# Optimization experiments

Hardware: AMD Instinct MI355X
Metric: run time of the kernel (lower is better)

Reference implementation:

```python
import jax, jax.numpy as jnp
import numpy as np

B, T, N, C = 1, 8, 1152, 768
H, DH = 12, 64          # attention heads / head dim; also RG-LRU block-diagonal heads
MLP = 3072
LRU = 768
CONV_W = 4              # recurrentgemma temporal conv width
N_IMG = 1024            # image tokens blocked by mask_image2image


def rms_norm(x, scale):
    var = jnp.mean(jnp.square(x), axis=-1, keepdims=True)
    return x * jax.lax.rsqrt(var + 1e-6) * (1.0 + scale)


def layer_norm(x, scale, bias):
    m = jnp.mean(x, axis=-1, keepdims=True)
    v = jnp.var(x, axis=-1, keepdims=True)
    return (x - m) * jax.lax.rsqrt(v + 1e-6) * scale + bias


def block_diag_linear(x, w, b):
    # x [..., LRU] -> per-head block-diagonal linear (recurrentgemma BlockDiagonalLinear)
    xs = x.reshape(x.shape[:-1] + (H, DH))
    y = jnp.einsum('...hd,hde->...he', xs, w) + b
    return y.reshape(x.shape)


def setup_inputs():
    key = jax.random.key(0)
    ks = jax.random.split(key, 24)
    def nrm(k, shape, s=0.02):
        return jax.random.normal(k, shape, jnp.float32) * s
    return dict(
        x=jax.random.normal(ks[0], (B, T, N, C), jnp.float32),
        tpre_scale=nrm(ks[1], (C,)),
        w_y=nrm(ks[2], (C, LRU)), b_y=jnp.zeros((LRU,)),
        w_x=nrm(ks[3], (C, LRU)), b_x=jnp.zeros((LRU,)),
        conv_w=nrm(ks[4], (CONV_W, LRU)), conv_b=jnp.zeros((LRU,)),
        a_param=jax.random.uniform(ks[5], (LRU,), jnp.float32, 1.0, 4.0),
        ig_w=nrm(ks[6], (H, DH, DH)), ig_b=jnp.zeros((H, DH)),
        ag_w=nrm(ks[7], (H, DH, DH)), ag_b=jnp.zeros((H, DH)),
        w_out=nrm(ks[8], (LRU, C)), b_out=jnp.zeros((C,)),
        cpre_scale=nrm(ks[9], (C,)),
        ffw_up_w=nrm(ks[10], (2, C, MLP)), ffw_up_b=jnp.zeros((2, MLP)),
        ffw_down_w=nrm(ks[11], (MLP, C)), ffw_down_b=jnp.zeros((C,)),
        ln1_s=jnp.ones((C,)), ln1_b=jnp.zeros((C,)),
        wq=nrm(ks[12], (C, H, DH)), bq=jnp.zeros((H, DH)),
        wk=nrm(ks[13], (C, H, DH)), bk=jnp.zeros((H, DH)),
        wv=nrm(ks[14], (C, H, DH)), bv=jnp.zeros((H, DH)),
        wo=nrm(ks[15], (H, DH, C)), bo=jnp.zeros((C,)),
        ln2_s=jnp.ones((C,)), ln2_b=jnp.zeros((C,)),
        mlp_w1=nrm(ks[16], (C, MLP)), mlp_b1=jnp.zeros((MLP,)),
        mlp_w2=nrm(ks[17], (MLP, C)), mlp_b2=jnp.zeros((C,)),
    )


def forward(x, tpre_scale, w_y, b_y, w_x, b_x, conv_w, conv_b, a_param,
            ig_w, ig_b, ag_w, ag_b, w_out, b_out, cpre_scale,
            ffw_up_w, ffw_up_b, ffw_down_w, ffw_down_b,
            ln1_s, ln1_b, wq, bq, wk, bk, wv, bv, wo, bo,
            ln2_s, ln2_b, mlp_w1, mlp_b1, mlp_w2, mlp_b2):
    b, t, n, c = x.shape
    # ---- temporal RG-LRU residual block over time: [(b t) n c] -> [(b n) t c] ----
    xt = x.transpose(0, 2, 1, 3).reshape(b * n, t, c)
    raw = xt
    xn = rms_norm(xt, tpre_scale)
    y = jax.nn.gelu(xn @ w_y + b_y)              # gate branch
    u = xn @ w_x + b_x                           # recurrent branch
    # causal depthwise temporal conv (width 4)
    up = jnp.pad(u, ((0, 0), (CONV_W - 1, 0), (0, 0)))
    u = sum(conv_w[i] * up[:, i:i + t] for i in range(CONV_W)) + conv_b
    # RG-LRU
    gate_x = jax.nn.sigmoid(block_diag_linear(u, ig_w, ig_b))
    gate_a = jax.nn.sigmoid(block_diag_linear(u, ag_w, ag_b))
    log_a = -8.0 * gate_a * jax.nn.softplus(a_param)
    a = jnp.exp(log_a)                           # [bn, t, LRU]
    mult = jnp.sqrt(jnp.maximum(1.0 - jnp.exp(2.0 * log_a), 0.0))
    reset = (jnp.arange(t) == 0)[None, :, None]
    mult = jnp.where(reset, 1.0, mult)
    a = jnp.where(reset, 0.0, a)
    norm_x = u * gate_x * mult
    def step(h, inputs):
        a_t, x_t = inputs
        h = a_t * h + x_t
        return h, h
    _, hs = jax.lax.scan(step, jnp.zeros((b * n, LRU), u.dtype),
                         (a.transpose(1, 0, 2), norm_x.transpose(1, 0, 2)))
    h = hs.transpose(1, 0, 2)                    # [bn, t, LRU]
    s = (h * y) @ w_out + b_out
    resid = s + raw
    # gated MLP (recurrentgemma MLPBlock)
    z = rms_norm(resid, cpre_scale)
    up2 = jnp.einsum('btd,cdD->cbtD', z, ffw_up_w) + ffw_up_b[:, None, None, :]
    z = (jax.nn.gelu(up2[0]) * up2[1]) @ ffw_down_w + ffw_down_b
    xt = z + resid
    # ---- spatial ViT block over tokens: back to [(b t) n c] ----
    xs = xt.reshape(b, n, t, c).transpose(0, 2, 1, 3).reshape(b * t, n, c)
    y1 = layer_norm(xs, ln1_s, ln1_b)
    q = jnp.einsum('bnc,chd->bnhd', y1, wq) + bq
    k = jnp.einsum('bnc,chd->bnhd', y1, wk) + bk
    v = jnp.einsum('bnc,chd->bnhd', y1, wv) + bv
    logits = jnp.einsum('bqhd,bkhd->bhqk', q, k) / jnp.sqrt(jnp.asarray(DH, q.dtype))
    # mask_image2image: image tokens (first 1024) cannot attend to image tokens
    mask = jnp.ones((n, n), bool).at[:N_IMG, :N_IMG].set(False)
    logits = jnp.where(mask[None, None], logits, jnp.finfo(logits.dtype).min)
    attn = jax.nn.softmax(logits, axis=-1)
    sa = jnp.einsum('bhqk,bkhd->bqhd', attn, v)
    sa = jnp.einsum('bqhd,hdc->bqc', sa, wo) + bo
    xs = xs + sa
    y2 = layer_norm(xs, ln2_s, ln2_b)
    m = jax.nn.gelu(y2 @ mlp_w1 + mlp_b1) @ mlp_w2 + mlp_b2
    xs = xs + m
    return xs.reshape(b, t, n, c)


def reference(x, tpre_scale, w_y, b_y, w_x, b_x, conv_w, conv_b, a_param,
              ig_w, ig_b, ag_w, ag_b, w_out, b_out, cpre_scale,
              ffw_up_w, ffw_up_b, ffw_down_w, ffw_down_b,
              ln1_s, ln1_b, wq, bq, wk, bk, wv, bv, wo, bo,
              ln2_s, ln2_b, mlp_w1, mlp_b1, mlp_w2, mlp_b2):
    return forward(x, tpre_scale, w_y, b_y, w_x, b_x, conv_w, conv_b, a_param,
                   ig_w, ig_b, ag_w, ag_b, w_out, b_out, cpre_scale,
                   ffw_up_w, ffw_up_b, ffw_down_w, ffw_down_b,
                   ln1_s, ln1_b, wq, bq, wk, bk, wv, bv, wo, bo,
                   ln2_s, ln2_b, mlp_w1, mlp_b1, mlp_w2, mlp_b2)
```

## Files before the change

### kernel.cpp

```cpp
#include <hip/hip_runtime.h>
#include <hip/hip_bf16.h>

typedef __hip_bfloat16 bf16;
typedef __attribute__((ext_vector_type(4))) float f32x4;
typedef __attribute__((ext_vector_type(8))) short short8;

#define T_ 8
#define N_ 1152
#define C_ 768
#define H_ 12
#define DH_ 64
#define MLP_ 3072
#define LRU_ 768
#define NIMG_ 1024
#define M_ (T_*N_)

__device__ __forceinline__ float b2f(bf16 v){ return __bfloat162float(v); }
__device__ __forceinline__ bf16  f2b(float f){ return __float2bfloat16(f); }
__device__ __forceinline__ float gelu_tanh(float x){
  float x3 = x*x*x;
  float z = 1.5957691216057308f*(x + 0.044715f*x3);
  float e = __expf(z);
  float t = 1.f - 2.f/(e + 1.f);
  return 0.5f*x*(1.f + t);
}
__device__ __forceinline__ void gll16(const void* g, void* l) {
  __builtin_amdgcn_global_load_lds((const __attribute__((address_space(1))) void*)g,
                                   (__attribute__((address_space(3))) void*)l, 16, 0, 0);
}
__device__ __forceinline__ f32x4 mfma16(short8 a, short8 b, f32x4 c) {
  return __builtin_amdgcn_mfma_f32_16x16x32_bf16(a, b, c, 0, 0, 0);
}

__global__ __launch_bounds__(256)
void convertT(const float* __restrict__ W, bf16* __restrict__ Wt, int Kd, int Nd,
              int rs, int ro) {
  __shared__ float tile[64][65];
  int k0 = blockIdx.y * 64, n0 = blockIdx.x * 64;
  int tid = threadIdx.x;
  int c = tid & 63, rr = tid >> 6;
  #pragma unroll
  for (int i = 0; i < 16; i++) {
    int r = rr * 16 + i;
    tile[r][c] = W[(size_t)(k0 + r) * Nd + n0 + c];
  }
  __syncthreads();
  #pragma unroll
  for (int i = 0; i < 16; i++) {
    int n = rr * 16 + i;
    Wt[(size_t)((n0 + n) * rs + ro) * Kd + k0 + c] = f2b(tile[c][n]);
  }
}

__global__ __launch_bounds__(256)
void convert_gw(const float* __restrict__ igw, const float* __restrict__ agw,
                const float* __restrict__ igb, const float* __restrict__ agb,
                bf16* __restrict__ GW, float* __restrict__ GB) {
  int h = blockIdx.x;
  for (int idx = threadIdx.x; idx < 128 * 64; idx += 256) {
    int rowc = idx >> 6;
    int d    = idx & 63;
    int e    = rowc >> 1;
    const float* W = (rowc & 1) ? agw : igw;
    GW[((size_t)h * 128 + rowc) * 64 + d] = f2b(W[((size_t)h * 64 + d) * 64 + e]);
  }
  if (threadIdx.x < 128) {
    int rowc = threadIdx.x;
    GB[h * 128 + rowc] = ((rowc & 1) ? agb : igb)[h * 64 + (rowc >> 1)];
  }
}

template<int EPI, int ACT>
__global__ __launch_bounds__(256)
void mgemm(const bf16* __restrict__ A, const bf16* __restrict__ Wt,
           const float* __restrict__ bias, const float* __restrict__ resid,
           void* __restrict__ outp, int K, int Nd) {
  __shared__ bf16 As[2][128][32];
  __shared__ bf16 Bs[2][128][32];
  int tid = threadIdx.x;
  int wave = tid >> 6, lane = tid & 63;
  int wm = wave >> 1, wn = wave & 1;
  int ln15 = lane & 15, quad = lane >> 4;
  int row0 = blockIdx.y * 128, col0 = blockIdx.x * 128;
  const bf16* ag = A  + (size_t)(row0 + wave*32 + (lane>>2)) * K + (lane&3)*8;
  const bf16* bg = Wt + (size_t)(col0 + wave*32 + (lane>>2)) * K + (lane&3)*8;
  f32x4 zero = {0.f, 0.f, 0.f, 0.f};
  f32x4 acc[4][4];
  #pragma unroll
  for (int i = 0; i < 4; i++)
    #pragma unroll
    for (int j = 0; j < 4; j++) acc[i][j] = zero;

  gll16(ag,          &As[0][wave*32][0]);
  gll16(ag + 16*K,   &As[0][wave*32 + 16][0]);
  gll16(bg,          &Bs[0][wave*32][0]);
  gll16(bg + 16*K,   &Bs[0][wave*32 + 16][0]);
  __syncthreads();

  int nt = K >> 5;
  int cur = 0;
  for (int t = 0; t < nt; ++t) {
    if (t + 1 < nt) {
      int k1 = (t + 1) << 5;
      gll16(ag + k1,          &As[cur^1][wave*32][0]);
      gll16(ag + 16*K + k1,   &As[cur^1][wave*32 + 16][0]);
      gll16(bg + k1,          &Bs[cur^1][wave*32][0]);
      gll16(bg + 16*K + k1,   &Bs[cur^1][wave*32 + 16][0]);
    }
    short8 af[4], bf[4];
    #pragma unroll
    for (int i = 0; i < 4; i++)
      af[i] = *(const short8*)&As[cur][wm*64 + i*16 + ln15][quad*8];
    #pragma unroll
    for (int i = 0; i < 4; i++)
      bf[i] = *(const short8*)&Bs[cur][wn*64 + i*16 + ln15][quad*8];
    #pragma unroll
    for (int i = 0; i < 4; i++)
      #pragma unroll
      for (int j = 0; j < 4; j++)
        acc[i][j] = mfma16(af[i], bf[j], acc[i][j]);
    __syncthreads();
    cur ^= 1;
  }

  #pragma unroll
  for (int i = 0; i < 4; i++) {
    #pragma unroll
    for (int j = 0; j < 4; j++) {
      int col = col0 + wn*64 + j*16 + ln15;
      float bv = (EPI == 3) ? bias[(col & 1) * (Nd >> 1) + (col >> 1)] : bias[col];
      #pragma unroll
      for (int r = 0; r < 4; r++) {
        int row = row0 + wm*64 + i*16 + quad*4 + r;
        float v = acc[i][j][r] + bv;
        if (EPI == 3) {
          float pv = __shfl_xor(v, 1, 64);
          if ((lane & 1) == 0)
            ((bf16*)outp)[(size_t)row * (Nd >> 1) + (col >> 1)] = f2b(gelu_tanh(v) * pv);
        } else {
          if (ACT) v = gelu_tanh(v);
          if (EPI == 0) {
            ((bf16*)outp)[(size_t)row * Nd + col] = f2b(v);
          } else if (EPI == 1) {
            size_t o = (size_t)row * Nd + col;
            ((float*)outp)[o] = v + resid[o];
          } else if (EPI == 2) {
            int tt = row / N_; int nn = row - tt * N_;
            ((bf16*)outp)[(((size_t)tt * H_ + (col >> 6)) * 64 + (col & 63)) * N_ + nn] = f2b(v);
          }
        }
      }
    }
  }
}

template<int LN>
__global__ __launch_bounds__(256)
void norm_kernel(const float* __restrict__ inp, const float* __restrict__ s,
                 const float* __restrict__ b, bf16* __restrict__ out) {
  int wid  = threadIdx.x >> 6;
  int lane = threadIdx.x & 63;
  int tok  = blockIdx.x * 4 + wid;
  float v[12];
  float sum = 0.f, sq = 0.f;
  #pragma unroll
  for (int i = 0; i < 12; i++) {
    int c = lane + i * 64;
    float x = inp[(size_t)tok*C_ + c];
    v[i] = x; sum += x; sq += x * x;
  }
  #pragma unroll
  for (int o = 32; o > 0; o >>= 1) {
    sum += __shfl_xor(sum, o, 64);
    sq  += __shfl_xor(sq, o, 64);
  }
  float scale, mean = 0.f;
  if (LN) {
    mean = sum * (1.f / C_);
    float var = sq * (1.f / C_) - mean * mean;
    scale = rsqrtf(var + 1e-6f);
  } else {
    scale = rsqrtf(sq * (1.f / C_) + 1e-6f);
  }
  #pragma unroll
  for (int i = 0; i < 12; i++) {
    int c = lane + i * 64;
    float sc = s[c];
    float r;
    if (LN) r = (v[i] - mean) * scale * sc + b[c];
    else    r = v[i] * scale * (1.f + sc);
    out[(size_t)tok*C_ + c] = f2b(r);
  }
}

__global__ __launch_bounds__(256)
void conv_kernel(const bf16* __restrict__ u0, const float* __restrict__ cw,
                 const float* __restrict__ cb, bf16* __restrict__ uc) {
  int idx = blockIdx.x * 256 + threadIdx.x;
  int ch  = idx % LRU_;
  int tok = idx / LRU_;
  int n = tok % N_;
  int t = tok / N_;
  float acc = cb[ch];
  #pragma unroll
  for (int i = 0; i < 4; i++) {
    int tt = t - 3 + i;
    if (tt >= 0)
      acc += cw[i*LRU_ + ch] * b2f(u0[(size_t)(tt*N_ + n)*LRU_ + ch]);
  }
  uc[idx] = f2b(acc);
}

__global__ __launch_bounds__(256)
void gates_mfma(const bf16* __restrict__ uc, const bf16* __restrict__ GW,
                const float* __restrict__ GB, const float* __restrict__ ap,
                bf16* __restrict__ a_out, bf16* __restrict__ nx_out) {
  __shared__ bf16 As[128][64];
  __shared__ bf16 Bs[128][64];
  int tid = threadIdx.x;
  int wave = tid >> 6, lane = tid & 63;
  int wm = wave >> 1, wn = wave & 1;
  int ln15 = lane & 15, quad = lane >> 4;
  int row0 = blockIdx.x * 128;
  int h = blockIdx.y;
  #pragma unroll
  for (int i = 0; i < 4; i++) {
    int chunk = wave * 4 + i;
    gll16(uc + (size_t)(row0 + chunk*8 + (lane>>3)) * LRU_ + h*DH_ + (lane&7)*8,
          &As[chunk*8][0]);
    gll16(GW + (size_t)h*128*64 + chunk*512 + lane*8, &Bs[chunk*8][0]);
  }
  __syncthreads();
  f32x4 zero = {0.f, 0.f, 0.f, 0.f};
  f32x4 acc[4][4];
  #pragma unroll
  for (int i = 0; i < 4; i++)
    #pragma unroll
    for (int j = 0; j < 4; j++) acc[i][j] = zero;
  short8 af0[4], af1[4], bf0[4], bf1[4];
  #pragma unroll
  for (int i = 0; i < 4; i++) {
    af0[i] = *(const short8*)&As[wm*64 + i*16 + ln15][quad*8];
    af1[i] = *(const short8*)&As[wm*64 + i*16 + ln15][32 + quad*8];
    bf0[i] = *(const short8*)&Bs[wn*64 + i*16 + ln15][quad*8];
    bf1[i] = *(const short8*)&Bs[wn*64 + i*16 + ln15][32 + quad*8];
  }
  #pragma unroll
  for (int i = 0; i < 4; i++)
    #pragma unroll
    for (int j = 0; j < 4; j++) {
      acc[i][j] = mfma16(af0[i], bf0[j], acc[i][j]);
      acc[i][j] = mfma16(af1[i], bf1[j], acc[i][j]);
    }
  __syncthreads();

  int t_is0 = (row0 < N_);
  int odd = lane & 1;
  float bvj[4], spj[4];
  #pragma unroll
  for (int j = 0; j < 4; j++) {
    int col = wn*64 + j*16 + ln15;
    bvj[j] = GB[h*128 + col];
    int e = col >> 1;
    float apv = ap[h*DH_ + e];
    spj[j] = (apv > 20.f) ? apv : log1pf(__expf(apv));
  }
  #pragma unroll
  for (int i = 0; i < 4; i++) {
    #pragma unroll
    for (int j = 0; j < 4; j++) {
      int col = wn*64 + j*16 + ln15;
      int e = col >> 1;
      #pragma unroll
      for (int r = 0; r < 4; r++) {
        int lr = wm*64 + i*16 + quad*4 + r;
        float v = acc[i][j][r] + bvj[j];
        float g = 1.f / (1.f + __expf(-v));
        float mult = 1.f;
        if (odd) {
          float log_a = -8.f * g * spj[j];
          float a = __expf(log_a);
          mult = sqrtf(fmaxf(1.f - a*a, 0.f));
          if (t_is0) { a = 0.f; mult = 1.f; }
          Bs[lr][e] = f2b(a);
        }
        float mp = __shfl_xor(mult, 1, 64);
        if (!odd) {
          float uv = b2f(As[lr][e]);
          As[lr][e] = f2b(uv * g * mp);
        }
      }
    }
  }
  __syncthreads();
  int rr = tid >> 3, cc = (tid & 7) * 8;
  #pragma unroll
  for (int it = 0; it < 4; it++) {
    int row = it * 32 + rr;
    size_t o = (size_t)(row0 + row) * LRU_ + h*DH_ + cc;
    *(short8*)(nx_out + o) = *(const short8*)&As[row][cc];
    *(short8*)(a_out  + o) = *(const short8*)&Bs[row][cc];
  }
}

__global__ __launch_bounds__(256)
void scan_kernel(const bf16* __restrict__ a, const bf16* __restrict__ nx,
                 const bf16* __restrict__ y, bf16* __restrict__ hy) {
  int idx = blockIdx.x * 256 + threadIdx.x;
  int n  = idx / LRU_;
  int ch = idx % LRU_;
  float h = 0.f;
  #pragma unroll
  for (int t = 0; t < T_; t++) {
    size_t p = (size_t)(t*N_ + n) * LRU_ + ch;
    h = b2f(a[p]) * h + b2f(nx[p]);
    hy[p] = f2b(h * b2f(y[p]));
  }
}

__global__ __launch_bounds__(256)
void fattn(const bf16* __restrict__ Q, const bf16* __restrict__ Kg,
           const bf16* __restrict__ Vt, bf16* __restrict__ O) {
  __shared__ bf16 Ks[128][64];
  __shared__ bf16 VTs[64][128];
  __shared__ bf16 Ps[4][16][128];
  int qb = blockIdx.x, th = blockIdx.y;
  int h = th % H_, t = th / H_;
  int wave = threadIdx.x >> 6, lane = threadIdx.x & 63;
  int ln15 = lane & 15, quad = lane >> 4;
  int q0, kv0, nch;
  if (qb < 16) { q0 = qb * 64;            kv0 = NIMG_; nch = 1; }
  else         { q0 = NIMG_ + (qb-16)*64; kv0 = 0;     nch = 9; }
  int qw = q0 + wave * 16;
  const bf16* qp = Q + (size_t)(t*N_ + qw + ln15) * C_ + h*DH_ + quad*8;
  short8 aq0 = *(const short8*)qp;
  short8 aq1 = *(const short8*)(qp + 32);
  f32x4 zero = {0.f, 0.f, 0.f, 0.f};
  f32x4 oacc[4];
  #pragma unroll
  for (int d = 0; d < 4; d++) oacc[d] = zero;
  float mi[4], li[4];
  #pragma unroll
  for (int r = 0; r < 4; r++) { mi[r] = -1e30f; li[r] = 0.f; }

  for (int ch = 0; ch < nch; ch++) {
    int kb = t*N_ + kv0 + ch*128;
    #pragma unroll
    for (int i = 0; i < 4; i++) {
      int r = wave*32 + i*8;
      gll16(Kg + (size_t)(kb + r + (lane>>3))*C_ + h*DH_ + (lane&7)*8, &Ks[r][0]);
    }
    #pragma unroll
    for (int i = 0; i < 4; i++) {
      int d = wave*16 + i*4;
      gll16(Vt + ((size_t)(t*H_ + h)*64 + d + (lane>>4))*N_ + kv0 + ch*128 + ln15*8,
            &VTs[d][0]);
    }
    __syncthreads();
    f32x4 s[8];
    #pragma unroll
    for (int nt = 0; nt < 8; nt++) {
      short8 b0 = *(const short8*)&Ks[nt*16 + ln15][quad*8];
      short8 b1 = *(const short8*)&Ks[nt*16 + ln15][32 + quad*8];
      f32x4 c_ = zero;
      c_ = mfma16(aq0, b0, c_);
      c_ = mfma16(aq1, b1, c_);
      #pragma unroll
      for (int r = 0; r < 4; r++) s[nt][r] = c_[r] * 0.125f;
    }
    float alpha[4], lsum[4];
    #pragma unroll
    for (int r = 0; r < 4; r++) {
      float m_ = s[0][r];
      #pragma unroll
      for (int nt = 1; nt < 8; nt++) m_ = fmaxf(m_, s[nt][r]);
      #pragma unroll
      for (int o = 1; o < 16; o <<= 1) m_ = fmaxf(m_, __shfl_xor(m_, o, 64));
      float mnew = fmaxf(mi[r], m_);
      alpha[r] = __expf(mi[r] - mnew);
      mi[r] = mnew;
      lsum[r] = 0.f;
    }
    #pragma unroll
    for (int nt = 0; nt < 8; nt++)
      #pragma unroll
      for (int r = 0; r < 4; r++) {
        float p = __expf(s[nt][r] - mi[r]);
        s[nt][r] = p; lsum[r] += p;
      }
    #pragma unroll
    for (int r = 0; r < 4; r++) {
      float l_ = lsum[r];
      #pragma unroll
      for (int o = 1; o < 16; o <<= 1) l_ += __shfl_xor(l_, o, 64);
      li[r] = li[r] * alpha[r] + l_;
    }
    #pragma unroll
    for (int nt = 0; nt < 8; nt++)
      #pragma unroll
      for (int r = 0; r < 4; r++)
        Ps[wave][quad*4 + r][nt*16 + ln15] = f2b(s[nt][r]);
    #pragma unroll
    for (int d = 0; d < 4; d++)
      #pragma unroll
      for (int r = 0; r < 4; r++) oacc[d][r] *= alpha[r];
    #pragma unroll
    for (int ks = 0; ks < 4; ks++) {
      short8 pa = *(const short8*)&Ps[wave][ln15][ks*32 + quad*8];
      #pragma unroll
      for (int dt = 0; dt < 4; dt++) {
        short8 vb = *(const short8*)&VTs[dt*16 + ln15][ks*32 + quad*8];
        oacc[dt] = mfma16(pa, vb, oacc[dt]);
      }
    }
    __syncthreads();
  }
  #pragma unroll
  for (int dt = 0; dt < 4; dt++)
    #pragma unroll
    for (int r = 0; r < 4; r++)
      O[(size_t)(t*N_ + qw + quad*4 + r)*C_ + h*DH_ + dt*16 + ln15]
        = f2b(oacc[dt][r] / li[r]);
}

extern "C" void kernel_launch(void* const* d_in, const int* in_sizes, int n_in,
                              void* d_out, int out_size, void* d_ws, size_t ws_size,
                              hipStream_t stream) {
  (void)in_sizes; (void)n_in; (void)out_size; (void)ws_size;
  const float* x        = (const float*)d_in[0];
  const float* tpre     = (const float*)d_in[1];
  const float* w_y      = (const float*)d_in[2];
  const float* b_y      = (const float*)d_in[3];
  const float* w_x      = (const float*)d_in[4];
  const float* b_x      = (const float*)d_in[5];
  const float* conv_w   = (const float*)d_in[6];
  const float* conv_b   = (const float*)d_in[7];
  const float* a_param  = (const float*)d_in[8];
  const float* ig_w     = (const float*)d_in[9];
  const float* ig_b     = (const float*)d_in[10];
  const float* ag_w     = (const float*)d_in[11];
  const float* ag_b     = (const float*)d_in[12];
  const float* w_out    = (const float*)d_in[13];
  const float* b_out    = (const float*)d_in[14];
  const float* cpre     = (const float*)d_in[15];
  const float* ffw_up_w = (const float*)d_in[16];
  const float* ffw_up_b = (const float*)d_in[17];
  const float* ffw_dn_w = (const float*)d_in[18];
  const float* ffw_dn_b = (const float*)d_in[19];
  const float* ln1_s    = (const float*)d_in[20];
  const float* ln1_b    = (const float*)d_in[21];
  const float* wq       = (const float*)d_in[22];
  const float* bq       = (const float*)d_in[23];
  const float* wk       = (const float*)d_in[24];
  const float* bk       = (const float*)d_in[25];
  const float* wv       = (const float*)d_in[26];
  const float* bv       = (const float*)d_in[27];
  const float* wo       = (const float*)d_in[28];
  const float* bo       = (const float*)d_in[29];
  const float* ln2_s    = (const float*)d_in[30];
  const float* ln2_b    = (const float*)d_in[31];
  const float* mlp_w1   = (const float*)d_in[32];
  const float* mlp_b1   = (const float*)d_in[33];
  const float* mlp_w2   = (const float*)d_in[34];
  const float* mlp_b2   = (const float*)d_in[35];

  const size_t MC = (size_t)M_ * C_;
  const size_t W68 = (size_t)C_ * C_;
  const size_t WUP = (size_t)C_ * MLP_;
  bf16* B0 = (bf16*)d_ws;
  bf16* B1 = B0 + MC;
  bf16* B2 = B1 + MC;
  bf16* BV = B2 + MC;
  float* F0 = (float*)(BV + MC);
  float* F1 = F0 + MC;
  bf16* F0b = (bf16*)F0;
  bf16* B0b = (bf16*)B0;
  float* xsF = (float*)B0;
  float* outF = (float*)d_out;
  bf16*  GW = (bf16*)F1;
  float* GB = (float*)(GW + (size_t)H_*128*64);

  dim3 blk(256);
  dim3 gN768(C_/128, M_/128);
  dim3 cv768(12, 12);
  dim3 cvUp(48, 12);
  dim3 cvDn(12, 48);

  convertT<<<cv768, blk, 0, stream>>>(w_y, BV, C_, C_, 1, 0);
  convertT<<<cv768, blk, 0, stream>>>(w_x, BV + W68, C_, C_, 1, 0);
  convert_gw<<<H_, blk, 0, stream>>>(ig_w, ag_w, ig_b, ag_b, GW, GB);
  norm_kernel<0><<<M_/4, blk, 0, stream>>>(x, tpre, nullptr, B0);
  mgemm<0,1><<<gN768, blk, 0, stream>>>(B0, BV, b_y, nullptr, B1, C_, C_);
  mgemm<0,0><<<gN768, blk, 0, stream>>>(B0, BV + W68, b_x, nullptr, B2, C_, C_);
  conv_kernel<<<(M_*LRU_)/256, blk, 0, stream>>>(B2, conv_w, conv_b, B0);
  gates_mfma<<<dim3(M_/128, H_), blk, 0, stream>>>(B0, GW, GB, a_param, B2, BV);
  scan_kernel<<<(N_*LRU_)/256, blk, 0, stream>>>(B2, BV, B1, B0);
  convertT<<<cv768, blk, 0, stream>>>(w_out, BV, C_, C_, 1, 0);
  mgemm<1,0><<<gN768, blk, 0, stream>>>(B0, BV, b_out, x, outF, C_, C_);

  norm_kernel<0><<<M_/4, blk, 0, stream>>>(outF, cpre, nullptr, B0);
  convertT<<<cvUp, blk, 0, stream>>>(ffw_up_w,       B1, C_, MLP_, 2, 0);
  convertT<<<cvUp, blk, 0, stream>>>(ffw_up_w + WUP, B1, C_, MLP_, 2, 1);
  convertT<<<cvDn, blk, 0, stream>>>(ffw_dn_w, BV, MLP_, C_, 1, 0);
  {
    dim3 gUp(6144/128, M_/128);
    dim3 gDn(C_/128,   M_/128);
    mgemm<3,0><<<gUp, blk, 0, stream>>>(B0, B1, ffw_up_b, nullptr, F0b, C_, 6144);
    mgemm<1,0><<<gDn, blk, 0, stream>>>(F0b, BV, ffw_dn_b, outF, xsF, MLP_, C_);
  }

  norm_kernel<1><<<M_/4, blk, 0, stream>>>(xsF, ln1_s, ln1_b, B2);
  convertT<<<cv768, blk, 0, stream>>>(wq, BV,          C_, C_, 1, 0);
  convertT<<<cv768, blk, 0, stream>>>(wk, BV + W68,    C_, C_, 1, 0);
  convertT<<<cv768, blk, 0, stream>>>(wv, BV + 2*W68,  C_, C_, 1, 0);
  convertT<<<cv768, blk, 0, stream>>>(wo, BV + 3*W68,  C_, C_, 1, 0);
  mgemm<0,0><<<gN768, blk, 0, stream>>>(B2, BV,         bq, nullptr, F0b,        C_, C_);
  mgemm<0,0><<<gN768, blk, 0, stream>>>(B2, BV + W68,   bk, nullptr, F0b + MC,   C_, C_);
  mgemm<2,0><<<gN768, blk, 0, stream>>>(B2, BV + 2*W68, bv, nullptr, F0b + 2*MC, C_, C_);
  fattn<<<dim3(18, T_*H_), blk, 0, stream>>>(F0b, F0b + MC, F0b + 2*MC, B2);
  mgemm<1,0><<<gN768, blk, 0, stream>>>(B2, BV + 3*W68, bo, xsF, outF, C_, C_);
  norm_kernel<1><<<M_/4, blk, 0, stream>>>(outF, ln2_s, ln2_b, B2);
  convertT<<<cvUp, blk, 0, stream>>>(mlp_w1, B0b,       C_, MLP_, 1, 0);
  convertT<<<cvDn, blk, 0, stream>>>(mlp_w2, B0b + WUP, MLP_, C_, 1, 0);
  {
    dim3 gM1(MLP_/128, M_/128);
    dim3 gM2(C_/128,   M_/128);
    mgemm<0,1><<<gM1, blk, 0, stream>>>(B2, B0b, mlp_b1, nullptr, F0b, C_, MLP_);
    mgemm<1,0><<<gM2, blk, 0, stream>>>(F0b, B0b + WUP, mlp_b2, outF, outF, MLP_, C_);
  }
}
```

Measured before the change: 928.6 us.

## Fuse paired GEMMs and weight conversions, vectorize norm, conv and scan kernels

Merges the y/x projection GEMMs and the q/k projection GEMMs into single N=1536 GEMMs with a split-bias epilogue, and batches several weight transposes into one multi-job launch via blockIdx.z. Norm, conv and scan kernels now process 4 or 8 channels per thread using vector loads and stores. fattn reads Q and K from the interleaved 1536-wide buffer. This cuts launch count and improves memory coalescing, at the cost of more buffer aliasing and stride bookkeeping.

```diff
diff --git a/kernel.cpp b/kernel.cpp
--- a/kernel.cpp
+++ b/kernel.cpp
@@ -4,6 +4,7 @@
 typedef __hip_bfloat16 bf16;
 typedef __attribute__((ext_vector_type(4))) float f32x4;
 typedef __attribute__((ext_vector_type(8))) short short8;
+typedef __attribute__((ext_vector_type(4))) short s16x4;
 
 #define T_ 8
 #define N_ 1152
@@ -17,6 +18,7 @@
 
 __device__ __forceinline__ float b2f(bf16 v){ return __bfloat162float(v); }
 __device__ __forceinline__ bf16  f2b(float f){ return __float2bfloat16(f); }
+__device__ __forceinline__ float bfs(short u){ return __uint_as_float(((unsigned int)(unsigned short)u) << 16); }
 __device__ __forceinline__ float gelu_tanh(float x){
   float x3 = x*x*x;
   float z = 1.5957691216057308f*(x + 0.044715f*x3);
@@ -36,6 +38,31 @@
 void convertT(const float* __restrict__ W, bf16* __restrict__ Wt, int Kd, int Nd,
               int rs, int ro) {
   __shared__ float tile[64][65];
+  int k0 = blockIdx.y * 64, n0 = blockIdx.x * 64;
+  int tid = threadIdx.x;
+  int c = tid & 63, rr = tid >> 6;
+  #pragma unroll
+  for (int i = 0; i < 16; i++) {
+    int r = rr * 16 + i;
+    tile[r][c] = W[(size_t)(k0 + r) * Nd + n0 + c];
+  }
+  __syncthreads();
+  #pragma unroll
+  for (int i = 0; i < 16; i++) {
+    int n = rr * 16 + i;
+    Wt[(size_t)((n0 + n) * rs + ro) * Kd + k0 + c] = f2b(tile[c][n]);
+  }
+}
+
+struct CvJob  { const float* src; bf16* dst; };
+struct CvJobs { CvJob j[4]; };
+__global__ __launch_bounds__(256)
+void convertT4(CvJobs jobs, int Kd, int Nd, int rs, int zro) {
+  __shared__ float tile[64][65];
+  int z = blockIdx.z;
+  const float* __restrict__ W  = jobs.j[z].src;
+  bf16* __restrict__ Wt        = jobs.j[z].dst;
+  int ro = z * zro;
   int k0 = blockIdx.y * 64, n0 = blockIdx.x * 64;
   int tid = threadIdx.x;
   int c = tid & 63, rr = tid >> 6;
@@ -73,7 +100,7 @@
 template<int EPI, int ACT>
 __global__ __launch_bounds__(256)
 void mgemm(const bf16* __restrict__ A, const bf16* __restrict__ Wt,
-           const float* __restrict__ bias, const float* __restrict__ resid,
+           const float* __restrict__ bias, const float* __restrict__ bias2,
            void* __restrict__ outp, int K, int Nd) {
   __shared__ bf16 As[2][128][32];
   __shared__ bf16 Bs[2][128][32];
@@ -128,7 +155,10 @@
     #pragma unroll
     for (int j = 0; j < 4; j++) {
       int col = col0 + wn*64 + j*16 + ln15;
-      float bv = (EPI == 3) ? bias[(col & 1) * (Nd >> 1) + (col >> 1)] : bias[col];
+      float bv;
+      if (EPI == 3)      bv = bias[(col & 1) * (Nd >> 1) + (col >> 1)];
+      else if (EPI == 4) bv = (col < (Nd >> 1)) ? bias[col] : bias2[col - (Nd >> 1)];
+      else               bv = bias[col];
       #pragma unroll
       for (int r = 0; r < 4; r++) {
         int row = row0 + wm*64 + i*16 + quad*4 + r;
@@ -137,13 +167,16 @@
           float pv = __shfl_xor(v, 1, 64);
           if ((lane & 1) == 0)
             ((bf16*)outp)[(size_t)row * (Nd >> 1) + (col >> 1)] = f2b(gelu_tanh(v) * pv);
+        } else if (EPI == 4) {
+          if (ACT && col < (Nd >> 1)) v = gelu_tanh(v);
+          ((bf16*)outp)[(size_t)row * Nd + col] = f2b(v);
         } else {
           if (ACT) v = gelu_tanh(v);
           if (EPI == 0) {
             ((bf16*)outp)[(size_t)row * Nd + col] = f2b(v);
           } else if (EPI == 1) {
             size_t o = (size_t)row * Nd + col;
-            ((float*)outp)[o] = v + resid[o];
+            ((float*)outp)[o] = v + bias2[o];
           } else if (EPI == 2) {
             int tt = row / N_; int nn = row - tt * N_;
             ((bf16*)outp)[(((size_t)tt * H_ + (col >> 6)) * 64 + (col & 63)) * N_ + nn] = f2b(v);
@@ -161,13 +194,14 @@
   int wid  = threadIdx.x >> 6;
   int lane = threadIdx.x & 63;
   int tok  = blockIdx.x * 4 + wid;
-  float v[12];
+  const float* ip = inp + (size_t)tok*C_ + lane*4;
+  f32x4 v[3];
   float sum = 0.f, sq = 0.f;
   #pragma unroll
-  for (int i = 0; i < 12; i++) {
-    int c = lane + i * 64;
-    float x = inp[(size_t)tok*C_ + c];
-    v[i] = x; sum += x; sq += x * x;
+  for (int i = 0; i < 3; i++) {
+    v[i] = *(const f32x4*)(ip + i*256);
+    #pragma unroll
+    for (int j = 0; j < 4; j++) { sum += v[i][j]; sq += v[i][j]*v[i][j]; }
   }
   #pragma unroll
   for (int o = 32; o > 0; o >>= 1) {
@@ -183,32 +217,57 @@
     scale = rsqrtf(sq * (1.f / C_) + 1e-6f);
   }
   #pragma unroll
-  for (int i = 0; i < 12; i++) {
-    int c = lane + i * 64;
-    float sc = s[c];
-    float r;
-    if (LN) r = (v[i] - mean) * scale * sc + b[c];
-    else    r = v[i] * scale * (1.f + sc);
-    out[(size_t)tok*C_ + c] = f2b(r);
+  for (int i = 0; i < 3; i++) {
+    int c0 = i*256 + lane*4;
+    f32x4 sc = *(const f32x4*)(s + c0);
+    f32x4 bb;
+    if (LN) bb = *(const f32x4*)(b + c0);
+    bf16 tmp[4];
+    #pragma unroll
+    for (int j = 0; j < 4; j++) {
+      float r;
+      if (LN) r = (v[i][j] - mean) * scale * sc[j] + bb[j];
+      else    r = v[i][j] * scale * (1.f + sc[j]);
+      tmp[j] = f2b(r);
+    }
+    *(s16x4*)(out + (size_t)tok*C_ + c0) = *(const s16x4*)tmp;
   }
 }
 
 __global__ __launch_bounds__(256)
 void conv_kernel(const bf16* __restrict__ u0, const float* __restrict__ cw,
-                 const float* __restrict__ cb, bf16* __restrict__ uc) {
+                 const float* __restrict__ cb, bf16* __restrict__ uc, int us, int uo) {
   int idx = blockIdx.x * 256 + threadIdx.x;
-  int ch  = idx % LRU_;
-  int tok = idx / LRU_;
+  int c8  = idx % (LRU_/8);
+  int tok = idx / (LRU_/8);
+  int ch0 = c8 * 8;
   int n = tok % N_;
   int t = tok / N_;
-  float acc = cb[ch];
+  float acc[8];
+  {
+    f32x4 b0 = *(const f32x4*)(cb + ch0);
+    f32x4 b1 = *(const f32x4*)(cb + ch0 + 4);
+    #pragma unroll
+    for (int j = 0; j < 4; j++) { acc[j] = b0[j]; acc[4+j] = b1[j]; }
+  }
   #pragma unroll
   for (int i = 0; i < 4; i++) {
     int tt = t - 3 + i;
-    if (tt >= 0)
-      acc += cw[i*LRU_ + ch] * b2f(u0[(size_t)(tt*N_ + n)*LRU_ + ch]);
-  }
-  uc[idx] = f2b(acc);
+    if (tt >= 0) {
+      short8 v = *(const short8*)&u0[(size_t)(tt*N_ + n)*us + uo + ch0];
+      f32x4 w0 = *(const f32x4*)(cw + i*LRU_ + ch0);
+      f32x4 w1 = *(const f32x4*)(cw + i*LRU_ + ch0 + 4);
+      #pragma unroll
+      for (int j = 0; j < 4; j++) {
+        acc[j]   += w0[j] * bfs(v[j]);
+        acc[4+j] += w1[j] * bfs(v[4+j]);
+      }
+    }
+  }
+  bf16 tmp[8];
+  #pragma unroll
+  for (int j = 0; j < 8; j++) tmp[j] = f2b(acc[j]);
+  *(short8*)&uc[(size_t)tok*LRU_ + ch0] = *(const short8*)tmp;
 }
 
 __global__ __launch_bounds__(256)
@@ -305,22 +364,31 @@
 
 __global__ __launch_bounds__(256)
 void scan_kernel(const bf16* __restrict__ a, const bf16* __restrict__ nx,
-                 const bf16* __restrict__ y, bf16* __restrict__ hy) {
+                 const bf16* __restrict__ y, bf16* __restrict__ hy, int ys) {
   int idx = blockIdx.x * 256 + threadIdx.x;
-  int n  = idx / LRU_;
-  int ch = idx % LRU_;
-  float h = 0.f;
+  int c8 = idx % (LRU_/8);
+  int n  = idx / (LRU_/8);
+  int ch0 = c8 * 8;
+  float h[8] = {0.f,0.f,0.f,0.f,0.f,0.f,0.f,0.f};
   #pragma unroll
   for (int t = 0; t < T_; t++) {
-    size_t p = (size_t)(t*N_ + n) * LRU_ + ch;
-    h = b2f(a[p]) * h + b2f(nx[p]);
-    hy[p] = f2b(h * b2f(y[p]));
-  }
-}
-
-__global__ __launch_bounds__(256)
-void fattn(const bf16* __restrict__ Q, const bf16* __restrict__ Kg,
-           const bf16* __restrict__ Vt, bf16* __restrict__ O) {
+    size_t p = (size_t)(t*N_ + n) * LRU_ + ch0;
+    short8 av = *(const short8*)(a + p);
+    short8 nv = *(const short8*)(nx + p);
+    short8 yv = *(const short8*)(y + (size_t)(t*N_ + n) * ys + ch0);
+    bf16 tmp[8];
+    #pragma unroll
+    for (int j = 0; j < 8; j++) {
+      h[j] = bfs(av[j]) * h[j] + bfs(nv[j]);
+      tmp[j] = f2b(h[j] * bfs(yv[j]));
+    }
+    *(short8*)(hy + p) = *(const short8*)tmp;
+  }
+}
+
+__global__ __launch_bounds__(256)
+void fattn(const bf16* __restrict__ QK, const bf16* __restrict__ Vt,
+           bf16* __restrict__ O) {
   __shared__ bf16 Ks[128][64];
   __shared__ bf16 VTs[64][128];
   __shared__ bf16 Ps[4][16][128];
@@ -332,7 +400,7 @@
   if (qb < 16) { q0 = qb * 64;            kv0 = NIMG_; nch = 1; }
   else         { q0 = NIMG_ + (qb-16)*64; kv0 = 0;     nch = 9; }
   int qw = q0 + wave * 16;
-  const bf16* qp = Q + (size_t)(t*N_ + qw + ln15) * C_ + h*DH_ + quad*8;
+  const bf16* qp = QK + (size_t)(t*N_ + qw + ln15) * 1536 + h*DH_ + quad*8;
   short8 aq0 = *(const short8*)qp;
   short8 aq1 = *(const short8*)(qp + 32);
   f32x4 zero = {0.f, 0.f, 0.f, 0.f};
@@ -348,7 +416,7 @@
     #pragma unroll
     for (int i = 0; i < 4; i++) {
       int r = wave*32 + i*8;
-      gll16(Kg + (size_t)(kb + r + (lane>>3))*C_ + h*DH_ + (lane&7)*8, &Ks[r][0]);
+      gll16(QK + (size_t)(kb + r + (lane>>3))*1536 + 768 + h*DH_ + (lane&7)*8, &Ks[r][0]);
     }
     #pragma unroll
     for (int i = 0; i < 4; i++) {
@@ -479,28 +547,31 @@
   float* outF = (float*)d_out;
   bf16*  GW = (bf16*)F1;
   float* GB = (float*)(GW + (size_t)H_*128*64);
+  bf16*  WtO = F0b + 3*MC;
 
   dim3 blk(256);
   dim3 gN768(C_/128, M_/128);
-  dim3 cv768(12, 12);
+  dim3 g1536(1536/128, M_/128);
   dim3 cvUp(48, 12);
   dim3 cvDn(12, 48);
 
-  convertT<<<cv768, blk, 0, stream>>>(w_y, BV, C_, C_, 1, 0);
-  convertT<<<cv768, blk, 0, stream>>>(w_x, BV + W68, C_, C_, 1, 0);
+  {
+    CvJobs j1 = {{{w_y, BV}, {w_x, BV + W68}, {w_out, WtO}, {w_y, BV}}};
+    convertT4<<<dim3(12, 12, 3), blk, 0, stream>>>(j1, C_, C_, 1, 0);
+  }
   convert_gw<<<H_, blk, 0, stream>>>(ig_w, ag_w, ig_b, ag_b, GW, GB);
   norm_kernel<0><<<M_/4, blk, 0, stream>>>(x, tpre, nullptr, B0);
-  mgemm<0,1><<<gN768, blk, 0, stream>>>(B0, BV, b_y, nullptr, B1, C_, C_);
-  mgemm<0,0><<<gN768, blk, 0, stream>>>(B0, BV + W68, b_x, nullptr, B2, C_, C_);
-  conv_kernel<<<(M_*LRU_)/256, blk, 0, stream>>>(B2, conv_w, conv_b, B0);
-  gates_mfma<<<dim3(M_/128, H_), blk, 0, stream>>>(B0, GW, GB, a_param, B2, BV);
-  scan_kernel<<<(N_*LRU_)/256, blk, 0, stream>>>(B2, BV, B1, B0);
-  convertT<<<cv768, blk, 0, stream>>>(w_out, BV, C_, C_, 1, 0);
-  mgemm<1,0><<<gN768, blk, 0, stream>>>(B0, BV, b_out, x, outF, C_, C_);
+  mgemm<4,1><<<g1536, blk, 0, stream>>>(B0, BV, b_y, b_x, F0b, C_, 1536);
+  conv_kernel<<<(M_*(LRU_/8))/256, blk, 0, stream>>>(F0b, conv_w, conv_b, B1, 1536, 768);
+  gates_mfma<<<dim3(M_/128, H_), blk, 0, stream>>>(B1, GW, GB, a_param, B2, BV);
+  scan_kernel<<<(N_*(LRU_/8))/256, blk, 0, stream>>>(B2, BV, F0b, B0, 1536);
+  mgemm<1,0><<<gN768, blk, 0, stream>>>(B0, WtO, b_out, x, outF, C_, C_);
 
   norm_kernel<0><<<M_/4, blk, 0, stream>>>(outF, cpre, nullptr, B0);
-  convertT<<<cvUp, blk, 0, stream>>>(ffw_up_w,       B1, C_, MLP_, 2, 0);
-  convertT<<<cvUp, blk, 0, stream>>>(ffw_up_w + WUP, B1, C_, MLP_, 2, 1);
+  {
+    CvJobs j2 = {{{ffw_up_w, B1}, {ffw_up_w + WUP, B1}, {ffw_up_w, B1}, {ffw_up_w, B1}}};
+    convertT4<<<dim3(48, 12, 2), blk, 0, stream>>>(j2, C_, MLP_, 2, 1);
+  }
   convertT<<<cvDn, blk, 0, stream>>>(ffw_dn_w, BV, MLP_, C_, 1, 0);
   {
     dim3 gUp(6144/128, M_/128);
@@ -510,14 +581,13 @@
   }
 
   norm_kernel<1><<<M_/4, blk, 0, stream>>>(xsF, ln1_s, ln1_b, B2);
-  convertT<<<cv768, blk, 0, stream>>>(wq, BV,          C_, C_, 1, 0);
-  convertT<<<cv768, blk, 0, stream>>>(wk, BV + W68,    C_, C_, 1, 0);
-  convertT<<<cv768, blk, 0, stream>>>(wv, BV + 2*W68,  C_, C_, 1, 0);
-  convertT<<<cv768, blk, 0, stream>>>(wo, BV + 3*W68,  C_, C_, 1, 0);
-  mgemm<0,0><<<gN768, blk, 0, stream>>>(B2, BV,         bq, nullptr, F0b,        C_, C_);
-  mgemm<0,0><<<gN768, blk, 0, stream>>>(B2, BV + W68,   bk, nullptr, F0b + MC,   C_, C_);
+  {
+    CvJobs j3 = {{{wq, BV}, {wk, BV + W68}, {wv, BV + 2*W68}, {wo, BV + 3*W68}}};
+    convertT4<<<dim3(12, 12, 4), blk, 0, stream>>>(j3, C_, C_, 1, 0);
+  }
+  mgemm<4,0><<<g1536, blk, 0, stream>>>(B2, BV, bq, bk, F0b, C_, 1536);
   mgemm<2,0><<<gN768, blk, 0, stream>>>(B2, BV + 2*W68, bv, nullptr, F0b + 2*MC, C_, C_);
-  fattn<<<dim3(18, T_*H_), blk, 0, stream>>>(F0b, F0b + MC, F0b + 2*MC, B2);
+  fattn<<<dim3(18, T_*H_), blk, 0, stream>>>(F0b, F0b + 2*MC, B2);
   mgemm<1,0><<<gN768, blk, 0, stream>>>(B2, BV + 3*W68, bo, xsF, outF, C_, C_);
   norm_kernel<1><<<M_/4, blk, 0, stream>>>(outF, ln2_s, ln2_b, B2);
   convertT<<<cvUp, blk, 0, stream>>>(mlp_w1, B0b,       C_, MLP_, 1, 0);
```

Measured after the change: 906.7 us. 1.02x faster.
